# Kernel tuning notes

Hardware: AMD Instinct MI355X
Metric: run time of the kernel (lower is better)

Reference implementation:

```python
import jax, jax.numpy as jnp
import numpy as np

N = 1_000_000   # query points
V = 1_000_000   # dual-octree vertices (feature table rows)
F = 32          # feature_dim

def setup_inputs() -> dict:
    key = jax.random.key(0)
    k1, k2, k3 = jax.random.split(key, 3)
    coeffs = jax.random.uniform(k1, (N, 8), dtype=jnp.float32)      # trilinear weights pre-clamp
    corner_idx = jax.random.randint(k2, (N, 8), 0, V, dtype=jnp.int64)  # trinkets[pidx]
    features = jax.random.normal(k3, (V, F), dtype=jnp.float32) * 0.01  # feature table (feature_std init)
    return {"coeffs": coeffs, "corner_idx": corner_idx, "features": features}

def reference(coeffs, corner_idx, features):
    # coeffs: [N,8], corner_idx: [N,8] -> gather [N,8,F], weighted sum over the 8 corners.
    c = jnp.clip(coeffs, 0.0, 1.0)              # torch.clamp(coeffs, 0, 1)
    feats = features[corner_idx]                # [N,8,F] irregular gather
    out = jnp.einsum('nk,nkf->nf', c, feats)    # (coeffs[...,None]*feats).sum(-2)
    return out
```

## Files before the change

kernel.cpp:

```cpp
#include <hip/hip_runtime.h>


constexpr int F = 32;
constexpr int QUERIES_PER_BLOCK = 32;

__global__ __launch_bounds__(256) void SPC_85469849190654_kernel(
    const float* __restrict__ coeffs,
    const int*   __restrict__ corner_idx,
    const float* __restrict__ features,
    float*       __restrict__ out,
    int N)
{
    __shared__ int   s_idx[256];
    __shared__ float s_c[256];

    const int t  = threadIdx.x;
    const int q0 = blockIdx.x * QUERIES_PER_BLOCK;

    const long long load_pos = (long long)q0 * 8 + t;
    if (load_pos < (long long)N * 8) {
        s_idx[t] = corner_idx[load_pos];
        s_c[t]   = coeffs[load_pos];
    } else {
        s_idx[t] = 0;
        s_c[t]   = 0.0f;
    }
    __syncthreads();

    const int q_local = t >> 3;
    const int g       = t & 7;
    const int n       = q0 + q_local;
    if (n >= N) return;

    const int   qbase = q_local << 3;
    const float* fb   = features + (g << 2);

    const float4 f0 = *reinterpret_cast<const float4*>(fb + (size_t)s_idx[qbase + 0] * F);
    const float4 f1 = *reinterpret_cast<const float4*>(fb + (size_t)s_idx[qbase + 1] * F);
    const float4 f2 = *reinterpret_cast<const float4*>(fb + (size_t)s_idx[qbase + 2] * F);
    const float4 f3 = *reinterpret_cast<const float4*>(fb + (size_t)s_idx[qbase + 3] * F);
    const float4 f4 = *reinterpret_cast<const float4*>(fb + (size_t)s_idx[qbase + 4] * F);
    const float4 f5 = *reinterpret_cast<const float4*>(fb + (size_t)s_idx[qbase + 5] * F);
    const float4 f6 = *reinterpret_cast<const float4*>(fb + (size_t)s_idx[qbase + 6] * F);
    const float4 f7 = *reinterpret_cast<const float4*>(fb + (size_t)s_idx[qbase + 7] * F);

    float4 acc = make_float4(0.f, 0.f, 0.f, 0.f);
    #define ACC(FK, K)                                             \
    {                                                              \
        float c = s_c[qbase + K];                                  \
        c = fminf(fmaxf(c, 0.0f), 1.0f);                           \
        acc.x = fmaf(c, FK.x, acc.x);                              \
        acc.y = fmaf(c, FK.y, acc.y);                              \
        acc.z = fmaf(c, FK.z, acc.z);                              \
        acc.w = fmaf(c, FK.w, acc.w);                              \
    }
    ACC(f0, 0) ACC(f1, 1) ACC(f2, 2) ACC(f3, 3)
    ACC(f4, 4) ACC(f5, 5) ACC(f6, 6) ACC(f7, 7)
    #undef ACC

    *reinterpret_cast<float4*>(out + (size_t)n * F + (g << 2)) = acc;
}

extern "C" void kernel_launch(void* const* d_in, const int* in_sizes, int n_in,
                              void* d_out, int out_size, void* d_ws, size_t ws_size,
                              hipStream_t stream) {
    const float* coeffs     = (const float*)d_in[0];
    const int*   corner_idx = (const int*)d_in[1];
    const float* features   = (const float*)d_in[2];
    float*       out        = (float*)d_out;

    const int N = in_sizes[0] / 8;
    const int blocks = (N + QUERIES_PER_BLOCK - 1) / QUERIES_PER_BLOCK;

    SPC_85469849190654_kernel<<<blocks, 256, 0, stream>>>(
        coeffs, corner_idx, features, out, N);
}
```

Measured before the change: 362.8 us.

## Convert feature table to fp16 in workspace and gather half-precision rows

Adds a pre-pass kernel that converts the fp32 feature table to fp16 in the workspace, and a gather kernel that reads 8-byte half4 chunks and accumulates in fp32. Output is written with nontemporal stores. The goal is to halve the bytes moved by the random gather, and a half-size table (64 MB) is more likely to stay in cache. The cost is an extra conversion pass over the full table on every call, plus fp16 rounding of the features. The fp32 path remains as a fallback when the workspace is too small.

```diff
diff --git a/kernel.cpp b/kernel.cpp
--- a/kernel.cpp
+++ b/kernel.cpp
@@ -4,7 +4,88 @@
 constexpr int F = 32;
 constexpr int QUERIES_PER_BLOCK = 32;
 
-__global__ __launch_bounds__(256) void SPC_85469849190654_kernel(
+typedef float    floatx4 __attribute__((ext_vector_type(4)));
+typedef _Float16 halfx8  __attribute__((ext_vector_type(8)));
+typedef _Float16 halfx4  __attribute__((ext_vector_type(4)));
+
+__global__ __launch_bounds__(256) void SPC_85469849190654_convert(
+    const float* __restrict__ features,
+    _Float16*    __restrict__ feat_h,
+    int total)
+{
+    const int i = (blockIdx.x * 256 + threadIdx.x) * 8;
+    if (i < total) {
+        const float4 a = *reinterpret_cast<const float4*>(features + i);
+        const float4 b = *reinterpret_cast<const float4*>(features + i + 4);
+        halfx8 h;
+        h[0] = (_Float16)a.x; h[1] = (_Float16)a.y;
+        h[2] = (_Float16)a.z; h[3] = (_Float16)a.w;
+        h[4] = (_Float16)b.x; h[5] = (_Float16)b.y;
+        h[6] = (_Float16)b.z; h[7] = (_Float16)b.w;
+        *reinterpret_cast<halfx8*>(feat_h + i) = h;
+    }
+}
+
+__global__ __launch_bounds__(256) void SPC_85469849190654_kernel_h(
+    const float*    __restrict__ coeffs,
+    const int*      __restrict__ corner_idx,
+    const _Float16* __restrict__ feat_h,
+    float*          __restrict__ out,
+    int N)
+{
+    __shared__ int   s_idx[256];
+    __shared__ float s_c[256];
+
+    const int t  = threadIdx.x;
+    const int q0 = blockIdx.x * QUERIES_PER_BLOCK;
+
+    const long long load_pos = (long long)q0 * 8 + t;
+    if (load_pos < (long long)N * 8) {
+        s_idx[t] = corner_idx[load_pos];
+        s_c[t]   = coeffs[load_pos];
+    } else {
+        s_idx[t] = 0;
+        s_c[t]   = 0.0f;
+    }
+    __syncthreads();
+
+    const int q_local = t >> 3;
+    const int g       = t & 7;
+    const int n       = q0 + q_local;
+    if (n >= N) return;
+
+    const int qbase = q_local << 3;
+    const _Float16* fb = feat_h + (g << 2);
+
+    const halfx4 h0 = *reinterpret_cast<const halfx4*>(fb + (size_t)s_idx[qbase + 0] * F);
+    const halfx4 h1 = *reinterpret_cast<const halfx4*>(fb + (size_t)s_idx[qbase + 1] * F);
+    const halfx4 h2 = *reinterpret_cast<const halfx4*>(fb + (size_t)s_idx[qbase + 2] * F);
+    const halfx4 h3 = *reinterpret_cast<const halfx4*>(fb + (size_t)s_idx[qbase + 3] * F);
+    const halfx4 h4 = *reinterpret_cast<const halfx4*>(fb + (size_t)s_idx[qbase + 4] * F);
+    const halfx4 h5 = *reinterpret_cast<const halfx4*>(fb + (size_t)s_idx[qbase + 5] * F);
+    const halfx4 h6 = *reinterpret_cast<const halfx4*>(fb + (size_t)s_idx[qbase + 6] * F);
+    const halfx4 h7 = *reinterpret_cast<const halfx4*>(fb + (size_t)s_idx[qbase + 7] * F);
+
+    float4 acc = make_float4(0.f, 0.f, 0.f, 0.f);
+    #define ACC(HK, K)                                             \
+    {                                                              \
+        float c = s_c[qbase + K];                                  \
+        c = fminf(fmaxf(c, 0.0f), 1.0f);                           \
+        acc.x = fmaf(c, (float)HK[0], acc.x);                      \
+        acc.y = fmaf(c, (float)HK[1], acc.y);                      \
+        acc.z = fmaf(c, (float)HK[2], acc.z);                      \
+        acc.w = fmaf(c, (float)HK[3], acc.w);                      \
+    }
+    ACC(h0, 0) ACC(h1, 1) ACC(h2, 2) ACC(h3, 3)
+    ACC(h4, 4) ACC(h5, 5) ACC(h6, 6) ACC(h7, 7)
+    #undef ACC
+
+    floatx4 accv = {acc.x, acc.y, acc.z, acc.w};
+    __builtin_nontemporal_store(
+        accv, reinterpret_cast<floatx4*>(out + (size_t)n * F + (g << 2)));
+}
+
+__global__ __launch_bounds__(256) void SPC_85469849190654_kernel_f32(
     const float* __restrict__ coeffs,
     const int*   __restrict__ corner_idx,
     const float* __restrict__ features,
@@ -69,9 +150,20 @@
     const float* features   = (const float*)d_in[2];
     float*       out        = (float*)d_out;
 
-    const int N = in_sizes[0] / 8;
+    const int N     = in_sizes[0] / 8;
+    const int VF    = in_sizes[2];
     const int blocks = (N + QUERIES_PER_BLOCK - 1) / QUERIES_PER_BLOCK;
 
-    SPC_85469849190654_kernel<<<blocks, 256, 0, stream>>>(
-        coeffs, corner_idx, features, out, N);
+    const size_t need = (size_t)VF * sizeof(_Float16);
+    if (ws_size >= need) {
+        _Float16* feat_h = (_Float16*)d_ws;
+        const int conv_blocks = (VF / 8 + 255) / 256;
+        SPC_85469849190654_convert<<<conv_blocks, 256, 0, stream>>>(
+            features, feat_h, VF);
+        SPC_85469849190654_kernel_h<<<blocks, 256, 0, stream>>>(
+            coeffs, corner_idx, feat_h, out, N);
+    } else {
+        SPC_85469849190654_kernel_f32<<<blocks, 256, 0, stream>>>(
+            coeffs, corner_idx, features, out, N);
+    }
 }
```

After: 388.8 us. 7.2% more time.
